# Kernel optimization log

Hardware: AMD Instinct MI355X
Metric: run time of the kernel (lower is better)

## Reference

```python
import jax, jax.numpy as jnp
import numpy as np

# dims / hyperparams (mirror init_kwargs)
B, N, C, K = 256, 16000, 32, 64          # batch, samples, cochlear channels, gammatone taps
FS, FMIN, FMAX, BWF = 16000, 100.0, 8000.0, 1.0
WINDOW, STRIDE = 256, 128                # inner hair cell framing -> T = 124
ANS, HID, OUT = 10, 50, 10               # auditory-nerve fanout, bushy/ic hidden, AC out
BETA, THR = 0.95, 1.0                    # snn.Leaky(beta=0.95), threshold 1.0, subtract reset
AN_LO, AN_HI, AN_THR = 0.5, 1.5, 0.5     # an_range scales + AN firing threshold

# Heaviside spike with ATan surrogate gradient (snntorch default style)
@jax.custom_vjp
def spike(u):
    return (u > 0).astype(u.dtype)

def _spike_fwd(u):
    return spike(u), u

def _spike_bwd(u, g):
    return (g / (1.0 + (jnp.pi * u) ** 2),)

spike.defvjp(_spike_fwd, _spike_bwd)

def _gammatone_bank():
    # ERB-spaced 4th-order gammatone impulse responses, unit L2 norm. [C, K]
    def hz2erb(f):
        return 21.4 * np.log10(1.0 + 0.00437 * f)
    def erb2hz(e):
        return (10.0 ** (e / 21.4) - 1.0) / 0.00437
    cfs = erb2hz(np.linspace(hz2erb(FMIN), hz2erb(FMAX), C))
    b = BWF * 1.019 * 24.7 * (4.37 * cfs / 1000.0 + 1.0)
    t = np.arange(K) / FS
    ker = (t[None, :] ** 3) * np.exp(-2 * np.pi * b[:, None] * t[None, :]) \
          * np.cos(2 * np.pi * cfs[:, None] * t[None, :])
    ker = ker / (np.linalg.norm(ker, axis=1, keepdims=True) + 1e-12)
    return jnp.asarray(ker, jnp.float32)

def setup_inputs() -> dict:
    key = jax.random.key(0)
    k1, k2, k3, k4 = jax.random.split(key, 4)
    audio = jax.random.normal(k1, (B, N), dtype=jnp.float32)
    W_bushy = jax.random.normal(k2, (HID, C * ANS), dtype=jnp.float32) / np.sqrt(C * ANS)
    W_ic = jax.random.normal(k3, (HID, HID), dtype=jnp.float32) / np.sqrt(HID)
    W_ac = jax.random.normal(k4, (OUT, HID), dtype=jnp.float32) / np.sqrt(HID)
    return {"audio": audio, "gt_kernels": _gammatone_bank(),
            "W_bushy": W_bushy, "W_ic": W_ic, "W_ac": W_ac}

def reference(audio, gt_kernels, W_bushy, W_ic, W_ac):
    # Cochlear: gammatone filterbank, [B,1,N] conv [C,1,K] SAME -> [B,C,N]
    y = jax.lax.conv_general_dilated(audio[:, None, :], gt_kernels[:, None, :],
                                     window_strides=(1,), padding="SAME")
    # InnerHairCell: half-wave rectify + moving-average framing -> [B,C,T]
    y = jnp.maximum(y, 0.0)
    env = jax.lax.reduce_window(y, 0.0, jax.lax.add,
                                (1, 1, WINDOW), (1, 1, STRIDE), "VALID") / WINDOW
    frames = jnp.transpose(env, (2, 0, 1))  # [T,B,C]
    scales = jnp.linspace(AN_LO, AN_HI, ANS, dtype=jnp.float32)

    def lif(mem, cur):
        mem = BETA * mem + cur
        spk = spike(mem - THR)
        return spk, mem - THR * spk  # subtract reset

    def step(carry, x_t):  # x_t [B,C]
        mem_b, mem_ic, mem_ac = carry
        # AuditoryNerve: ans scaled copies per channel, threshold fire -> [B, C*ANS]
        spk_an = spike(x_t[:, :, None] * scales - AN_THR).reshape(x_t.shape[0], -1)
        spk_b, mem_b = lif(mem_b, spk_an @ W_bushy.T)     # Bushy
        spk_ic, mem_ic = lif(mem_ic, spk_b @ W_ic.T)      # InferiorColliculus
        spk_ac, mem_ac = lif(mem_ac, spk_ic @ W_ac.T)     # AudioCortex
        return (mem_b, mem_ic, mem_ac), (spk_ac, mem_ac)

    bsz = audio.shape[0]
    init = (jnp.zeros((bsz, HID), audio.dtype),
            jnp.zeros((bsz, HID), audio.dtype),
            jnp.zeros((bsz, OUT), audio.dtype))
    _, (spk_rec, mem_rec) = jax.lax.scan(step, init, frames)
    # stack along dim=1 as in torch code -> [B,T,OUT]
    return jnp.transpose(spk_rec, (1, 0, 2)), jnp.transpose(mem_rec, (1, 0, 2))
```

## Files before the change

### kernel.cpp

```cpp
#include <hip/hip_runtime.h>

#define B_   256
#define N_   16000
#define C_   32
#define K_   64
#define T_   124
#define NJ   125
#define HID_ 50
#define OUT_ 10
#define TB_  1024
#define CURS 52

typedef unsigned int u32;
typedef float v2f __attribute__((ext_vector_type(2)));
struct __align__(16) f2x2 { v2f lo, hi; };

__device__ __forceinline__ float fadd(float a, float b) { return __fadd_rn(a, b); }
__device__ __forceinline__ float fmul(float a, float b) { return __fmul_rn(a, b); }
__device__ __forceinline__ float fsub(float a, float b) { return __fsub_rn(a, b); }

__device__ __forceinline__ void PKFMA(v2f& y, v2f a, const f2x2& T, int k) {
    switch (k) {
    case 0:  asm("v_pk_fma_f32 %0, %1, %2, %0 op_sel:[0,0,0] op_sel_hi:[1,0,1]"
                 : "+v"(y) : "v"(a), "s"(T.lo)); break;
    case 1:  asm("v_pk_fma_f32 %0, %1, %2, %0 op_sel:[0,1,0] op_sel_hi:[1,1,1]"
                 : "+v"(y) : "v"(a), "s"(T.lo)); break;
    case 2:  asm("v_pk_fma_f32 %0, %1, %2, %0 op_sel:[0,0,0] op_sel_hi:[1,0,1]"
                 : "+v"(y) : "v"(a), "s"(T.hi)); break;
    default: asm("v_pk_fma_f32 %0, %1, %2, %0 op_sel:[0,1,0] op_sel_hi:[1,1,1]"
                 : "+v"(y) : "v"(a), "s"(T.hi)); break;
    }
}

__global__ __launch_bounds__(256, 6) void convA(const float* __restrict__ audio,
                                                const float* __restrict__ gt,
                                                float* __restrict__ Sg) {
    __shared__ __align__(16) float abI[1280];
    __shared__ __align__(16) float ybuf[4][4][264];

    const int b = blockIdx.x, g = blockIdx.y;
    const int tid = threadIdx.x, w = tid >> 6, lane = tid & 63;
    const float* arow = audio + (size_t)b * N_;

    const int origin = (g << 10) - 32;
    for (int idx = tid; idx < 1280; idx += 256) {
        int P = idx / 640, j = idx - P * 640;
        int ii = j >> 1, h = j & 1;
        int gi = origin + (P << 9) + (h << 8) + ii;
        float v = (gi >= 0 && gi < N_) ? arow[gi] : 0.0f;
        abI[P * 640 + (j ^ (((j >> 5) & 1) << 2))] = v;
    }
    __syncthreads();

    for (int G = 0; G < 2; ++G) {
        const int rowbase = __builtin_amdgcn_readfirstlane(((w << 3) + (G << 2)) << 6);
        const float* kg = gt + rowbase;

        v2f Y[2][4][4];
#pragma unroll
        for (int P = 0; P < 2; ++P)
#pragma unroll
            for (int ch = 0; ch < 4; ++ch)
#pragma unroll
                for (int d = 0; d < 4; ++d) { Y[P][ch][d].x = 0.0f; Y[P][ch][d].y = 0.0f; }

        {
            f2x2 Tc[4];
#pragma unroll
            for (int ch = 0; ch < 4; ++ch)
                Tc[ch] = *(const f2x2*)(kg + (ch << 6));
            const int u = lane;
            const int p1 = (u << 3) ^ (((u >> 2) & 1) << 2);
#pragma unroll
            for (int P = 0; P < 2; ++P) {
                const float* abP = abI + P * 640;
                const f2x2 A0 = *(const f2x2*)(abP + p1);
                const f2x2 A1 = *(const f2x2*)(abP + (p1 ^ 4));
#pragma unroll
                for (int e = 0; e < 4; ++e) {
                    const v2f a = (e == 0) ? A0.lo : (e == 1) ? A0.hi
                                : (e == 2) ? A1.lo : A1.hi;
#pragma unroll
                    for (int ch = 0; ch < 4; ++ch)
#pragma unroll
                        for (int d = 0; d < 4; ++d) {
                            const int kb = e - 1 - d;
                            if (kb >= 0) PKFMA(Y[P][ch][d], a, Tc[ch], kb);
                        }
                }
            }
        }

#pragma unroll 1
        for (int q = 1; q < 16; ++q) {
            f2x2 Tm[4], Tc[4];
#pragma unroll
            for (int ch = 0; ch < 4; ++ch) {
                Tm[ch] = *(const f2x2*)(kg + (ch << 6) + ((q - 1) << 2));
                Tc[ch] = *(const f2x2*)(kg + (ch << 6) + (q << 2));
            }
            const int u = lane + q;
            const int p1 = (u << 3) ^ (((u >> 2) & 1) << 2);
#pragma unroll
            for (int P = 0; P < 2; ++P) {
                const float* abP = abI + P * 640;
                const f2x2 A0 = *(const f2x2*)(abP + p1);
                const f2x2 A1 = *(const f2x2*)(abP + (p1 ^ 4));
#pragma unroll
                for (int e = 0; e < 4; ++e) {
                    const v2f a = (e == 0) ? A0.lo : (e == 1) ? A0.hi
                                : (e == 2) ? A1.lo : A1.hi;
#pragma unroll
                    for (int ch = 0; ch < 4; ++ch)
#pragma unroll
                        for (int d = 0; d < 4; ++d) {
                            const int ts = e - 1 - d;
                            if (ts >= 0) PKFMA(Y[P][ch][d], a, Tc[ch], ts);
                            else         PKFMA(Y[P][ch][d], a, Tm[ch], 4 + ts);
                        }
                }
            }
        }

        {
            f2x2 Tm[4];
#pragma unroll
            for (int ch = 0; ch < 4; ++ch)
                Tm[ch] = *(const f2x2*)(kg + (ch << 6) + 60);
            const int u = lane + 16;
            const int p1 = (u << 3) ^ (((u >> 2) & 1) << 2);
#pragma unroll
            for (int P = 0; P < 2; ++P) {
                const float* abP = abI + P * 640;
                const f2x2 A0 = *(const f2x2*)(abP + p1);
                const f2x2 A1 = *(const f2x2*)(abP + (p1 ^ 4));
#pragma unroll
                for (int e = 0; e < 4; ++e) {
                    const v2f a = (e == 0) ? A0.lo : (e == 1) ? A0.hi
                                : (e == 2) ? A1.lo : A1.hi;
#pragma unroll
                    for (int ch = 0; ch < 4; ++ch)
#pragma unroll
                        for (int d = 0; d < 4; ++d) {
                            const int ts = e - 1 - d;
                            if (ts < 0) PKFMA(Y[P][ch][d], a, Tm[ch], 4 + ts);
                        }
                }
            }
        }

#pragma unroll
        for (int pp = 0; pp < 4; ++pp) {
            const int P = pp >> 1, h = pp & 1;
#pragma unroll
            for (int ch = 0; ch < 4; ++ch) {
                float4 z;
                z.x = fmaxf(h ? Y[P][ch][0].y : Y[P][ch][0].x, 0.0f);
                z.y = fmaxf(h ? Y[P][ch][1].y : Y[P][ch][1].x, 0.0f);
                z.z = fmaxf(h ? Y[P][ch][2].y : Y[P][ch][2].x, 0.0f);
                z.w = fmaxf(h ? Y[P][ch][3].y : Y[P][ch][3].x, 0.0f);
                *(float4*)(&ybuf[w][ch][((lane >> 5) * 132) + ((lane & 31) << 2)]) = z;
            }
            {
                const int ch2 = lane >> 4, blk = (lane >> 3) & 1, j = lane & 7;
                const float* yb = &ybuf[w][ch2][blk * 132 + j];
                float r = yb[0];
#pragma unroll
                for (int m = 1; m < 16; ++m) r = fadd(r, yb[m << 3]);
                float v = fadd(r, __shfl_xor(r, 1));
                v = fadd(v, __shfl_xor(v, 2));
                v = fadd(v, __shfl_xor(v, 4));
                const int jg = (g << 3) + (pp << 1) + blk;
                const int c = (w << 3) + (G << 2) + ch2;
                if (j == 0 && jg < NJ) Sg[((size_t)b * C_ + c) * NJ + jg] = v;
            }
        }
    }
}

__global__ __launch_bounds__(TB_, 1) void snnB(const float* __restrict__ Sg,
                                               const float* __restrict__ Wb,
                                               const float* __restrict__ Wic,
                                               const float* __restrict__ Wac,
                                               float* __restrict__ out) {
    __shared__ float sWb[HID_ * 321];
    __shared__ __align__(16) float sWic[HID_ * 52];
    __shared__ __align__(16) float sWac[OUT_ * 52];
    __shared__ u32   mask[128 * 10];
    __shared__ __align__(16) float cur[T_ * CURS];
    __shared__ __align__(16) float icur[T_ * CURS];
    __shared__ float acur[T_ * 12];

    const int b = blockIdx.x, tid = threadIdx.x;

    for (int i = tid; i < HID_ * 320; i += TB_) {
        int r = i / 320;
        sWb[r * 321 + (i - r * 320)] = Wb[i];
    }
    for (int i = tid; i < HID_ * HID_; i += TB_) {
        int r = i / 50;
        sWic[r * 52 + (i - r * 50)] = Wic[i];
    }
    for (int i = tid; i < OUT_ * HID_; i += TB_) {
        int r = i / 50;
        sWac[r * 52 + (i - r * 50)] = Wac[i];
    }

    const float* Sb = Sg + (size_t)b * C_ * NJ;
    for (int idx = tid; idx < 1280; idx += TB_) {
        if (idx >= T_ * 10) { mask[idx] = 0; continue; }
        int t = idx / 10, wd = idx - t * 10;
        u32 m = 0;
        int c_prev = -1;
        float env = 0.0f;
        for (int k = 0; k < 32; ++k) {
            int i = wd * 32 + k;
            int c = i / 10, s = i - c * 10;
            if (c != c_prev) {
                env = fmul(fadd(Sb[c * NJ + t], Sb[c * NJ + t + 1]), 0.00390625f);
                c_prev = c;
            }
            float sf = (s == 9) ? 1.5f : (float)(0.5 + (double)s * (1.0 / 9.0));
            if (fsub(fmul(env, sf), 0.5f) > 0.0f) m |= (1u << k);
        }
        mask[idx] = m;
    }
    __syncthreads();

    if (tid < 16 * HID_) {
        const int t0 = tid / 50, h = tid - t0 * 50;
        const float* wr = sWb + h * 321;
        const u32* mrow = mask + t0 * 10;
        float a0 = 0.0f, a1 = 0.0f, a2 = 0.0f, a3 = 0.0f;
        float a4 = 0.0f, a5 = 0.0f, a6 = 0.0f, a7 = 0.0f;
#pragma unroll 1
        for (int wi = 0; wi < 10; ++wi) {
            const u32 w0 = mrow[wi], w1 = mrow[160 + wi];
            const u32 w2 = mrow[320 + wi], w3 = mrow[480 + wi];
            const u32 w4 = mrow[640 + wi], w5 = mrow[800 + wi];
            const u32 w6 = mrow[960 + wi], w7 = mrow[1120 + wi];
#pragma unroll
            for (int b2 = 0; b2 < 32; ++b2) {
                const float wv = wr[(wi << 5) + b2];
                const int iw = __float_as_int(wv);
                a0 = fadd(a0, __int_as_float(iw & __builtin_amdgcn_sbfe((int)w0, b2, 1)));
                a1 = fadd(a1, __int_as_float(iw & __builtin_amdgcn_sbfe((int)w1, b2, 1)));
                a2 = fadd(a2, __int_as_float(iw & __builtin_amdgcn_sbfe((int)w2, b2, 1)));
                a3 = fadd(a3, __int_as_float(iw & __builtin_amdgcn_sbfe((int)w3, b2, 1)));
                a4 = fadd(a4, __int_as_float(iw & __builtin_amdgcn_sbfe((int)w4, b2, 1)));
                a5 = fadd(a5, __int_as_float(iw & __builtin_amdgcn_sbfe((int)w5, b2, 1)));
                a6 = fadd(a6, __int_as_float(iw & __builtin_amdgcn_sbfe((int)w6, b2, 1)));
                a7 = fadd(a7, __int_as_float(iw & __builtin_amdgcn_sbfe((int)w7, b2, 1)));
            }
        }
        cur[(t0      ) * CURS + h] = a0;
        cur[(t0 + 16 ) * CURS + h] = a1;
        cur[(t0 + 32 ) * CURS + h] = a2;
        cur[(t0 + 48 ) * CURS + h] = a3;
        cur[(t0 + 64 ) * CURS + h] = a4;
        cur[(t0 + 80 ) * CURS + h] = a5;
        cur[(t0 + 96 ) * CURS + h] = a6;
        if (t0 + 112 < T_) cur[(t0 + 112) * CURS + h] = a7;
    }
    __syncthreads();

    if (tid < HID_) {
        float mem = 0.0f;
        for (int t = 0; t < T_; ++t) {
            float m = fadd(fmul(0.95f, mem), cur[t * CURS + tid]);
            float sp = (fsub(m, 1.0f) > 0.0f) ? 1.0f : 0.0f;
            mem = fsub(m, sp);
            cur[t * CURS + tid] = sp;
        }
    }
    __syncthreads();

    for (int idx = tid; idx < T_ * HID_; idx += TB_) {
        int t = idx / 50, h = idx - t * 50;
        const float* wr = sWic + h * 52;
        const float* sb = cur + t * CURS;
        float acc = 0.0f;
#pragma unroll
        for (int g4 = 0; g4 < 12; ++g4) {
            const float4 s4 = *(const float4*)(sb + (g4 << 2));
            const float4 w4 = *(const float4*)(wr + (g4 << 2));
            acc = fmaf(s4.x, w4.x, acc);
            acc = fmaf(s4.y, w4.y, acc);
            acc = fmaf(s4.z, w4.z, acc);
            acc = fmaf(s4.w, w4.w, acc);
        }
        acc = fmaf(sb[48], wr[48], acc);
        acc = fmaf(sb[49], wr[49], acc);
        icur[t * CURS + h] = acc;
    }
    __syncthreads();

    if (tid < HID_) {
        float mem = 0.0f;
        for (int t = 0; t < T_; ++t) {
            float m = fadd(fmul(0.95f, mem), icur[t * CURS + tid]);
            float sp = (fsub(m, 1.0f) > 0.0f) ? 1.0f : 0.0f;
            mem = fsub(m, sp);
            icur[t * CURS + tid] = sp;
        }
    }
    __syncthreads();

    for (int idx = tid; idx < T_ * OUT_; idx += TB_) {
        int t = idx / 10, o = idx - t * 10;
        const float* wr = sWac + o * 52;
        const float* sb = icur + t * CURS;
        float acc = 0.0f;
#pragma unroll
        for (int g4 = 0; g4 < 12; ++g4) {
            const float4 s4 = *(const float4*)(sb + (g4 << 2));
            const float4 w4 = *(const float4*)(wr + (g4 << 2));
            acc = fmaf(s4.x, w4.x, acc);
            acc = fmaf(s4.y, w4.y, acc);
            acc = fmaf(s4.z, w4.z, acc);
            acc = fmaf(s4.w, w4.w, acc);
        }
        acc = fmaf(sb[48], wr[48], acc);
        acc = fmaf(sb[49], wr[49], acc);
        acur[t * 12 + o] = acc;
    }
    __syncthreads();

    if (tid < OUT_) {
        float mem = 0.0f;
        for (int t = 0; t < T_; ++t) {
            float m = fadd(fmul(0.95f, mem), acur[t * 12 + tid]);
            float sp = (fsub(m, 1.0f) > 0.0f) ? 1.0f : 0.0f;
            float mo = fsub(m, sp);
            mem = mo;
            size_t base = ((size_t)b * T_ + t) * OUT_ + tid;
            out[base] = sp;
            out[(size_t)(B_ * T_ * OUT_) + base] = mo;
        }
    }
}

extern "C" void kernel_launch(void* const* d_in, const int* in_sizes, int n_in,
                              void* d_out, int out_size, void* d_ws, size_t ws_size,
                              hipStream_t stream) {
    (void)in_sizes; (void)n_in; (void)out_size; (void)ws_size;
    const float* audio = (const float*)d_in[0];
    const float* gt    = (const float*)d_in[1];
    const float* Wb    = (const float*)d_in[2];
    const float* Wic   = (const float*)d_in[3];
    const float* Wac   = (const float*)d_in[4];

    float* Sg = (float*)d_ws;

    convA<<<dim3(B_, 16), dim3(256), 0, stream>>>(audio, gt, Sg);
    snnB<<<dim3(B_), dim3(TB_), 0, stream>>>(Sg, Wb, Wic, Wac, (float*)d_out);
}
```

Baseline: 325.9 us.

## Tune conv occupancy and padding, batch LIF loads, pair outputs in SNN matvecs

```diff
diff --git a/kernel.cpp b/kernel.cpp
--- a/kernel.cpp
+++ b/kernel.cpp
@@ -32,11 +32,11 @@
     }
 }
 
-__global__ __launch_bounds__(256, 6) void convA(const float* __restrict__ audio,
+__global__ __launch_bounds__(256, 4) void convA(const float* __restrict__ audio,
                                                 const float* __restrict__ gt,
                                                 float* __restrict__ Sg) {
     __shared__ __align__(16) float abI[1280];
-    __shared__ __align__(16) float ybuf[4][4][264];
+    __shared__ __align__(16) float ybuf[4][4][272];
 
     const int b = blockIdx.x, g = blockIdx.y;
     const int tid = threadIdx.x, w = tid >> 6, lane = tid & 63;
@@ -159,11 +159,11 @@
                 z.y = fmaxf(h ? Y[P][ch][1].y : Y[P][ch][1].x, 0.0f);
                 z.z = fmaxf(h ? Y[P][ch][2].y : Y[P][ch][2].x, 0.0f);
                 z.w = fmaxf(h ? Y[P][ch][3].y : Y[P][ch][3].x, 0.0f);
-                *(float4*)(&ybuf[w][ch][((lane >> 5) * 132) + ((lane & 31) << 2)]) = z;
+                *(float4*)(&ybuf[w][ch][((lane >> 5) * 136) + ((lane & 31) << 2)]) = z;
             }
             {
                 const int ch2 = lane >> 4, blk = (lane >> 3) & 1, j = lane & 7;
-                const float* yb = &ybuf[w][ch2][blk * 132 + j];
+                const float* yb = &ybuf[w][ch2][blk * 136 + j];
                 float r = yb[0];
 #pragma unroll
                 for (int m = 1; m < 16; ++m) r = fadd(r, yb[m << 3]);
@@ -266,7 +266,19 @@
 
     if (tid < HID_) {
         float mem = 0.0f;
-        for (int t = 0; t < T_; ++t) {
+        for (int t0 = 0; t0 < 120; t0 += 8) {
+            float c0[8];
+#pragma unroll
+            for (int k = 0; k < 8; ++k) c0[k] = cur[(t0 + k) * CURS + tid];
+#pragma unroll
+            for (int k = 0; k < 8; ++k) {
+                float m = fadd(fmul(0.95f, mem), c0[k]);
+                float sp = (fsub(m, 1.0f) > 0.0f) ? 1.0f : 0.0f;
+                mem = fsub(m, sp);
+                cur[(t0 + k) * CURS + tid] = sp;
+            }
+        }
+        for (int t = 120; t < T_; ++t) {
             float m = fadd(fmul(0.95f, mem), cur[t * CURS + tid]);
             float sp = (fsub(m, 1.0f) > 0.0f) ? 1.0f : 0.0f;
             mem = fsub(m, sp);
@@ -275,29 +287,44 @@
     }
     __syncthreads();
 
-    for (int idx = tid; idx < T_ * HID_; idx += TB_) {
-        int t = idx / 50, h = idx - t * 50;
-        const float* wr = sWic + h * 52;
+    for (int idx = tid; idx < T_ * 25; idx += TB_) {
+        int t = idx / 25, hp = idx - t * 25;
+        const float* w0 = sWic + hp * 52;
+        const float* w1 = sWic + (hp + 25) * 52;
         const float* sb = cur + t * CURS;
-        float acc = 0.0f;
+        float acc0 = 0.0f, acc1 = 0.0f;
 #pragma unroll
         for (int g4 = 0; g4 < 12; ++g4) {
             const float4 s4 = *(const float4*)(sb + (g4 << 2));
-            const float4 w4 = *(const float4*)(wr + (g4 << 2));
-            acc = fmaf(s4.x, w4.x, acc);
-            acc = fmaf(s4.y, w4.y, acc);
-            acc = fmaf(s4.z, w4.z, acc);
-            acc = fmaf(s4.w, w4.w, acc);
-        }
-        acc = fmaf(sb[48], wr[48], acc);
-        acc = fmaf(sb[49], wr[49], acc);
-        icur[t * CURS + h] = acc;
+            const float4 wa = *(const float4*)(w0 + (g4 << 2));
+            const float4 wb = *(const float4*)(w1 + (g4 << 2));
+            acc0 = fmaf(s4.x, wa.x, acc0);  acc1 = fmaf(s4.x, wb.x, acc1);
+            acc0 = fmaf(s4.y, wa.y, acc0);  acc1 = fmaf(s4.y, wb.y, acc1);
+            acc0 = fmaf(s4.z, wa.z, acc0);  acc1 = fmaf(s4.z, wb.z, acc1);
+            acc0 = fmaf(s4.w, wa.w, acc0);  acc1 = fmaf(s4.w, wb.w, acc1);
+        }
+        acc0 = fmaf(sb[48], w0[48], acc0);  acc1 = fmaf(sb[48], w1[48], acc1);
+        acc0 = fmaf(sb[49], w0[49], acc0);  acc1 = fmaf(sb[49], w1[49], acc1);
+        icur[t * CURS + hp] = acc0;
+        icur[t * CURS + hp + 25] = acc1;
     }
     __syncthreads();
 
     if (tid < HID_) {
         float mem = 0.0f;
-        for (int t = 0; t < T_; ++t) {
+        for (int t0 = 0; t0 < 120; t0 += 8) {
+            float c0[8];
+#pragma unroll
+            for (int k = 0; k < 8; ++k) c0[k] = icur[(t0 + k) * CURS + tid];
+#pragma unroll
+            for (int k = 0; k < 8; ++k) {
+                float m = fadd(fmul(0.95f, mem), c0[k]);
+                float sp = (fsub(m, 1.0f) > 0.0f) ? 1.0f : 0.0f;
+                mem = fsub(m, sp);
+                icur[(t0 + k) * CURS + tid] = sp;
+            }
+        }
+        for (int t = 120; t < T_; ++t) {
             float m = fadd(fmul(0.95f, mem), icur[t * CURS + tid]);
             float sp = (fsub(m, 1.0f) > 0.0f) ? 1.0f : 0.0f;
             mem = fsub(m, sp);
@@ -306,29 +333,47 @@
     }
     __syncthreads();
 
-    for (int idx = tid; idx < T_ * OUT_; idx += TB_) {
-        int t = idx / 10, o = idx - t * 10;
-        const float* wr = sWac + o * 52;
+    for (int idx = tid; idx < T_ * 5; idx += TB_) {
+        int t = idx / 5, op = idx - t * 5;
+        const float* w0 = sWac + op * 52;
+        const float* w1 = sWac + (op + 5) * 52;
         const float* sb = icur + t * CURS;
-        float acc = 0.0f;
+        float acc0 = 0.0f, acc1 = 0.0f;
 #pragma unroll
         for (int g4 = 0; g4 < 12; ++g4) {
             const float4 s4 = *(const float4*)(sb + (g4 << 2));
-            const float4 w4 = *(const float4*)(wr + (g4 << 2));
-            acc = fmaf(s4.x, w4.x, acc);
-            acc = fmaf(s4.y, w4.y, acc);
-            acc = fmaf(s4.z, w4.z, acc);
-            acc = fmaf(s4.w, w4.w, acc);
-        }
-        acc = fmaf(sb[48], wr[48], acc);
-        acc = fmaf(sb[49], wr[49], acc);
-        acur[t * 12 + o] = acc;
+            const float4 wa = *(const float4*)(w0 + (g4 << 2));
+            const float4 wb = *(const float4*)(w1 + (g4 << 2));
+            acc0 = fmaf(s4.x, wa.x, acc0);  acc1 = fmaf(s4.x, wb.x, acc1);
+            acc0 = fmaf(s4.y, wa.y, acc0);  acc1 = fmaf(s4.y, wb.y, acc1);
+            acc0 = fmaf(s4.z, wa.z, acc0);  acc1 = fmaf(s4.z, wb.z, acc1);
+            acc0 = fmaf(s4.w, wa.w, acc0);  acc1 = fmaf(s4.w, wb.w, acc1);
+        }
+        acc0 = fmaf(sb[48], w0[48], acc0);  acc1 = fmaf(sb[48], w1[48], acc1);
+        acc0 = fmaf(sb[49], w0[49], acc0);  acc1 = fmaf(sb[49], w1[49], acc1);
+        acur[t * 12 + op] = acc0;
+        acur[t * 12 + op + 5] = acc1;
     }
     __syncthreads();
 
     if (tid < OUT_) {
         float mem = 0.0f;
-        for (int t = 0; t < T_; ++t) {
+        for (int t0 = 0; t0 < 120; t0 += 8) {
+            float c0[8];
+#pragma unroll
+            for (int k = 0; k < 8; ++k) c0[k] = acur[(t0 + k) * 12 + tid];
+#pragma unroll
+            for (int k = 0; k < 8; ++k) {
+                float m = fadd(fmul(0.95f, mem), c0[k]);
+                float sp = (fsub(m, 1.0f) > 0.0f) ? 1.0f : 0.0f;
+                float mo = fsub(m, sp);
+                mem = mo;
+                size_t base = ((size_t)b * T_ + (t0 + k)) * OUT_ + tid;
+                out[base] = sp;
+                out[(size_t)(B_ * T_ * OUT_) + base] = mo;
+            }
+        }
+        for (int t = 120; t < T_; ++t) {
             float m = fadd(fmul(0.95f, mem), acur[t * 12 + tid]);
             float sp = (fsub(m, 1.0f) > 0.0f) ? 1.0f : 0.0f;
             float mo = fsub(m, sp);
```

Result: faster. 309.1 us (-5.2%).
